# Kernel optimization log

Hardware: AMD Instinct MI355X
Metric: run time of the kernel (lower is better)

## Reference

```python
import jax, jax.numpy as jnp
import numpy as np

B, Hh, Ww, C = 2, 56, 56, 256
NH = 8
MH = MW = 7
NQ = 15


def setup_inputs() -> dict:
    key = jax.random.key(0)
    ks = jax.random.split(key, 8)
    x = jax.random.normal(ks[0], (B, Hh, Ww, C), jnp.float32)
    clstoken = jax.random.normal(ks[1], (B, NQ, C), jnp.float32)
    WN = MH * MW                      # 49 image windows
    WinPix = (Hh // MH) * (Ww // MW)  # 64 pixels per window
    clsWin = -(-NQ // WinPix)         # ceil -> 1 extra cls window
    M = WN + clsWin                   # 50
    # sparse top-k style routing mask; cls rows/cols all True (as in BiLayer)
    mask = jax.random.bernoulli(ks[2], 0.1, (B, M, M))
    mask = mask.at[:, WN:, :].set(True).at[:, :, WN:].set(True)
    mask = mask | jnp.eye(M, dtype=bool)[None]
    Wqkv = jax.random.normal(ks[3], (C, 3 * C), jnp.float32) * (C ** -0.5)
    bqkv = jnp.zeros((3 * C,), jnp.float32)
    lepe_w = jax.random.normal(ks[4], (3, 3, 1, C), jnp.float32) * 0.1  # depthwise HWIO
    lepe_b = jnp.zeros((C,), jnp.float32)
    Wo = jax.random.normal(ks[5], (C, C), jnp.float32) * (C ** -0.5)
    bo = jnp.zeros((C,), jnp.float32)
    return dict(x=x, clstoken=clstoken, mask=mask, Wqkv=Wqkv, bqkv=bqkv,
                lepe_w=lepe_w, lepe_b=lepe_b, Wo=Wo, bo=bo, mask_h=MH, mask_w=MW)


def reference(x, clstoken, mask, Wqkv, bqkv, lepe_w, lepe_b, Wo, bo, mask_h, mask_w):
    Bb, H, W, Cc = x.shape
    Nq = clstoken.shape[1]
    Nh = NH
    Hd = Cc // Nh
    Win_h, Win_w = H // mask_h, W // mask_w
    WinPix = Win_h * Win_w
    S_img = H * W
    S = S_img + Nq
    scale = Cc ** -0.5

    qkv = x @ Wqkv + bqkv
    q, k, v = jnp.split(qkv, 3, axis=-1)
    qkv_c = clstoken @ Wqkv + bqkv
    qc, kc, vc = jnp.split(qkv_c, 3, axis=-1)

    # depthwise lepe conv on v (NHWC)
    lepe = jax.lax.conv_general_dilated(
        v, lepe_w, (1, 1), 'SAME',
        dimension_numbers=('NHWC', 'HWIO', 'NHWC'),
        feature_group_count=Cc) + lepe_b

    def win(t):  # [B,H,W,C] -> [B,Nh,(j i h w),Hd] window-major token order
        t = t.reshape(Bb, mask_h, Win_h, mask_w, Win_w, Nh, Hd)
        return t.transpose(0, 5, 1, 3, 2, 4, 6).reshape(Bb, Nh, S_img, Hd)

    def heads_c(t):  # [B,Nq,C] -> [B,Nh,Nq,Hd]
        return t.reshape(Bb, Nq, Nh, Hd).transpose(0, 2, 1, 3)

    q = jnp.concatenate([win(q), heads_c(qc)], axis=2)
    k = jnp.concatenate([win(k), heads_c(kc)], axis=2)
    v = jnp.concatenate([win(v), heads_c(vc)], axis=2)

    # token-level mask from window-level routing mask: mask[b, q//WinPix, kv//WinPix]
    win_id = jnp.arange(S) // WinPix
    tokmask = mask[:, win_id[:, None], win_id[None, :]]  # [B,S,S]

    logits = jnp.einsum('bnqd,bnkd->bnqk', q, k) * scale
    logits = jnp.where(tokmask[:, None], logits, jnp.float32(-1e9))
    attn = jax.nn.softmax(logits, axis=-1)
    out = jnp.einsum('bnqk,bnkd->bnqd', attn, v)

    cls_out = out[:, :, S_img:, :].transpose(0, 2, 1, 3).reshape(Bb, Nq, Cc)
    ximg = out[:, :, :S_img, :].reshape(Bb, Nh, mask_h, mask_w, Win_h, Win_w, Hd)
    ximg = ximg.transpose(0, 2, 4, 3, 5, 1, 6).reshape(Bb, H, W, Cc)

    x_out = (ximg + lepe) @ Wo + bo
    cls_out = cls_out @ Wo + bo
    return (x_out, cls_out)
```

## Files before the change

kernel.cpp:

```cpp
#include <hip/hip_runtime.h>
#include <hip/hip_bf16.h>
#include <math.h>

#define Bsz 2
#define NHd 8
#define HD 32
#define CC 256
#define Himg 56
#define Wimg 56
#define SIMG 3136
#define NQtok 15
#define SS 3151
#define SP 3200
#define NWIN 50
#define WN 49
#define MM 50
#define MROWS (Bsz*SP)
#define NROWS (Bsz*SS)

#define QSZ (Bsz*NHd*SP*HD)
#define VSPSZ (Bsz*SIMG*CC)
#define ASZ (MROWS*CC)
#define WTSZ (768*CC)
#define WOTSZ (CC*CC)
#define USZ (MROWS*CC)

typedef __attribute__((ext_vector_type(8))) short bf16x8;
typedef __attribute__((ext_vector_type(4))) float f32x4;

__device__ __forceinline__ short f2bf(float f) {
    __hip_bfloat16 h = __float2bfloat16(f);
    return *reinterpret_cast<short*>(&h);
}
__device__ __forceinline__ float bf2f(short s) {
    unsigned int u = ((unsigned int)(unsigned short)s) << 16;
    return __uint_as_float(u);
}

__global__ __launch_bounds__(256) void prep_all(
        const float* __restrict__ x, const float* __restrict__ cls,
        const float* __restrict__ Wqkv, const float* __restrict__ Wo,
        const unsigned char* __restrict__ raw,
        short* __restrict__ Abf, short* __restrict__ Wt, short* __restrict__ Wot,
        unsigned char* __restrict__ mask8) {
    __shared__ __align__(16) float tile[64][65];
    int bid = blockIdx.x;
    int tid = threadIdx.x;
    if (bid < 800) {
        int idx = bid * 256 + tid;
        int row = idx >> 5;
        int c8 = (idx & 31) * 8;
        int b = row / SP, tok = row % SP;
        bf16x8 o = {0, 0, 0, 0, 0, 0, 0, 0};
        const float* p = nullptr;
        if (tok < SIMG)      p = x + (long)(b * SIMG + tok) * CC + c8;
        else if (tok < SS)   p = cls + (long)(b * NQtok + tok - SIMG) * CC + c8;
        if (p) {
            float4 a = *(const float4*)p, bb = *(const float4*)(p + 4);
            o[0] = f2bf(a.x); o[1] = f2bf(a.y); o[2] = f2bf(a.z); o[3] = f2bf(a.w);
            o[4] = f2bf(bb.x); o[5] = f2bf(bb.y); o[6] = f2bf(bb.z); o[7] = f2bf(bb.w);
        }
        *(bf16x8*)(Abf + (long)row * CC + c8) = o;
    } else if (bid < 864) {
        const float* src; short* dst; int srcld, k0, n0;
        if (bid < 848) {
            int b2 = bid - 800;
            k0 = (b2 & 3) * 64; n0 = (b2 >> 2) * 64;
            src = Wqkv; srcld = 768; dst = Wt;
        } else {
            int b2 = bid - 848;
            k0 = (b2 & 3) * 64; n0 = (b2 >> 2) * 64;
            src = Wo; srcld = 256; dst = Wot;
        }
        int c = tid & 63, r0 = tid >> 6;
        #pragma unroll
        for (int p = 0; p < 16; p++) {
            int kl = p * 4 + r0;
            tile[kl][c] = src[(long)(k0 + kl) * srcld + n0 + c];
        }
        __syncthreads();
        #pragma unroll
        for (int p = 0; p < 16; p++) {
            int nl = p * 4 + r0;
            dst[(long)(n0 + nl) * CC + k0 + c] = f2bf(tile[c][nl]);
        }
    } else {
        __shared__ int type_s;
        if (tid == 0) {
            int isbool = (raw[2453] | raw[2457] | raw[2461]) != 0;
            if (isbool) type_s = 0;
            else {
                unsigned int wd = *(const unsigned int*)(raw + 9800);
                type_s = (wd == 0x3F800000u) ? 2 : 1;
            }
        }
        __syncthreads();
        int t = type_s;
        for (int i = tid; i < Bsz * MM * MM; i += 256) {
            unsigned char v;
            if (t == 0) v = raw[i] ? 1 : 0;
            else v = (*(const unsigned int*)(raw + 4 * i)) ? 1 : 0;
            mask8[i] = v;
        }
    }
}

__global__ __launch_bounds__(256, 2) void qkv_gemm_mfma(
        const short* __restrict__ Abf, const short* __restrict__ Wt,
        const float* __restrict__ bqkv,
        short* __restrict__ Qbf, short* __restrict__ Kbf, short* __restrict__ Vtb,
        short* __restrict__ Vsp) {
    int tid = threadIdx.x;
    int w = tid >> 6, l = tid & 63, l15 = l & 15, hi = l >> 4;
    int row0 = blockIdx.x * 128 + w * 32;
    int n0 = blockIdx.y * 64;
    f32x4 acc[2][4];
    #pragma unroll
    for (int rs = 0; rs < 2; rs++)
        #pragma unroll
        for (int t = 0; t < 4; t++) acc[rs][t] = (f32x4){0.f, 0.f, 0.f, 0.f};
    const short* Ap0 = Abf + (long)(row0 + l15) * CC + hi * 8;
    const short* Ap1 = Ap0 + 16 * CC;
    const short* Bp = Wt + (long)(n0 + l15) * CC + hi * 8;
    #pragma unroll
    for (int k0 = 0; k0 < 256; k0 += 32) {
        bf16x8 a0 = *(const bf16x8*)(Ap0 + k0);
        bf16x8 a1 = *(const bf16x8*)(Ap1 + k0);
        #pragma unroll
        for (int t = 0; t < 4; t++) {
            bf16x8 bf = *(const bf16x8*)(Bp + t * 16 * CC + k0);
            acc[0][t] = __builtin_amdgcn_mfma_f32_16x16x32_bf16(a0, bf, acc[0][t], 0, 0, 0);
            acc[1][t] = __builtin_amdgcn_mfma_f32_16x16x32_bf16(a1, bf, acc[1][t], 0, 0, 0);
        }
    }
    float bias[4];
    #pragma unroll
    for (int t = 0; t < 4; t++) bias[t] = bqkv[n0 + t * 16 + l15];
    int which = n0 >> 8;
    #pragma unroll
    for (int rs = 0; rs < 2; rs++) {
        #pragma unroll
        for (int r = 0; r < 4; r++) {
            int row = row0 + rs * 16 + hi * 4 + r;
            int b = row / SP, tok = row % SP;
            int s;
            if (tok < SIMG) {
                int h = tok / Wimg, wq = tok % Wimg;
                s = (((h >> 3) * 7 + (wq >> 3)) << 6) | ((h & 7) << 3) | (wq & 7);
            } else s = tok;
            #pragma unroll
            for (int t = 0; t < 4; t++) {
                int n = n0 + t * 16 + l15;
                float v = acc[rs][t][r] + bias[t];
                int cch = n & 255;
                int head = cch >> 5, d = cch & 31;
                long off = (((long)(b * NHd + head)) * SP + s) * HD + d;
                if (which == 0)      Qbf[off] = f2bf(v * 0.0625f);
                else if (which == 1) Kbf[off] = f2bf(v);
                else {
                    short vb = f2bf(v);
                    Vtb[(((long)(b * NHd + head)) * NWIN + (s >> 6)) * 2048
                        + d * 64 + (s & 63)] = vb;
                    if (tok < SIMG) Vsp[(long)(b * SIMG + tok) * CC + cch] = vb;
                }
            }
        }
    }
}

__global__ __launch_bounds__(256, 2) void attn_mfma(
        const short* __restrict__ Qbf, const short* __restrict__ Kbf,
        const short* __restrict__ Vtb, const short* __restrict__ Vsp,
        const float* __restrict__ lepe_w, const float* __restrict__ lepe_b,
        const unsigned char* __restrict__ mask8,
        short* __restrict__ U) {
    __shared__ __align__(16) short Pl[4][16][72];
    __shared__ float Ms[4][16], Ls[4][16];
    __shared__ float MAcc[4][16][32];

    int qb = blockIdx.x % NWIN;
    int bh = blockIdx.x / NWIN;
    int b = bh >> 3, head = bh & 7;
    int tid = threadIdx.x;
    int w = tid >> 6;
    int l = tid & 63;
    int l15 = l & 15;
    int hi = l >> 4;
    bool is_cls = (qb == WN);
    int qrow0 = is_cls ? 0 : w * 16;

    bf16x8 qf = *(const bf16x8*)&Qbf[((long)bh * SP + qb * 64 + qrow0 + l15) * HD + hi * 8];

    f32x4 acc0 = {0.f, 0.f, 0.f, 0.f};
    f32x4 acc1 = {0.f, 0.f, 0.f, 0.f};
    float m_run[4], l_run[4];
    #pragma unroll
    for (int r = 0; r < 4; r++) { m_run[r] = -1e30f; l_run[r] = 0.f; }

    unsigned long long bits;
    if (!is_cls) {
        const unsigned char* mrow = mask8 + ((long)b * MM + qb) * MM;
        bits = __ballot(l < NWIN && mrow[l] != 0);
    } else {
        bits = (0x1111111111111ULL << w) & ((1ULL << 50) - 1);
    }

    int kb = __builtin_ctzll(bits);
    bits &= bits - 1;
    const short* Kp = Kbf + ((long)bh * SP + kb * 64) * HD + hi * 8;
    bf16x8 kc0 = *(const bf16x8*)(Kp + (0 * 16 + l15) * HD);
    bf16x8 kc1 = *(const bf16x8*)(Kp + (1 * 16 + l15) * HD);
    bf16x8 kc2 = *(const bf16x8*)(Kp + (2 * 16 + l15) * HD);
    bf16x8 kc3 = *(const bf16x8*)(Kp + (3 * 16 + l15) * HD);

    for (;;) {
        long kbase = ((long)bh * SP + kb * 64) * HD;
        const short* Vp = Vtb + kbase;
        bf16x8 va = *(const bf16x8*)&Vp[l15 * 64 + hi * 8];
        bf16x8 vb = *(const bf16x8*)&Vp[(16 + l15) * 64 + hi * 8];
        bf16x8 vc = *(const bf16x8*)&Vp[l15 * 64 + 32 + hi * 8];
        bf16x8 vd = *(const bf16x8*)&Vp[(16 + l15) * 64 + 32 + hi * 8];

        f32x4 s[4];
        {
            f32x4 z = {0.f, 0.f, 0.f, 0.f};
            s[0] = __builtin_amdgcn_mfma_f32_16x16x32_bf16(qf, kc0, z, 0, 0, 0);
            s[1] = __builtin_amdgcn_mfma_f32_16x16x32_bf16(qf, kc1, z, 0, 0, 0);
            s[2] = __builtin_amdgcn_mfma_f32_16x16x32_bf16(qf, kc2, z, 0, 0, 0);
            s[3] = __builtin_amdgcn_mfma_f32_16x16x32_bf16(qf, kc3, z, 0, 0, 0);
        }
        if (kb == WN) {
            #pragma unroll
            for (int t = 0; t < 4; t++)
                if (t * 16 + l15 >= NQtok) { s[t][0] = s[t][1] = s[t][2] = s[t][3] = -1e30f; }
        }

        int nkb = -1;
        bf16x8 kn0, kn1, kn2, kn3;
        if (bits) {
            nkb = __builtin_ctzll(bits);
            bits &= bits - 1;
            const short* Kn = Kbf + ((long)bh * SP + nkb * 64) * HD + hi * 8;
            kn0 = *(const bf16x8*)(Kn + (0 * 16 + l15) * HD);
            kn1 = *(const bf16x8*)(Kn + (1 * 16 + l15) * HD);
            kn2 = *(const bf16x8*)(Kn + (2 * 16 + l15) * HD);
            kn3 = *(const bf16x8*)(Kn + (3 * 16 + l15) * HD);
        }

        #pragma unroll
        for (int r = 0; r < 4; r++) {
            float pm = fmaxf(fmaxf(s[0][r], s[1][r]), fmaxf(s[2][r], s[3][r]));
            pm = fmaxf(pm, __shfl_xor(pm, 1));
            pm = fmaxf(pm, __shfl_xor(pm, 2));
            pm = fmaxf(pm, __shfl_xor(pm, 4));
            pm = fmaxf(pm, __shfl_xor(pm, 8));
            float mn = fmaxf(m_run[r], pm);
            float alpha = __expf(m_run[r] - mn);
            float ps = 0.f;
            #pragma unroll
            for (int t = 0; t < 4; t++) {
                float p = __expf(s[t][r] - mn);
                s[t][r] = p;
                ps += p;
            }
            ps += __shfl_xor(ps, 1);
            ps += __shfl_xor(ps, 2);
            ps += __shfl_xor(ps, 4);
            ps += __shfl_xor(ps, 8);
            l_run[r] = l_run[r] * alpha + ps;
            m_run[r] = mn;
            acc0[r] *= alpha;
            acc1[r] *= alpha;
            #pragma unroll
            for (int t = 0; t < 4; t++)
                Pl[w][hi * 4 + r][t * 16 + l15] = f2bf(s[t][r]);
        }
        bf16x8 pa0 = *(const bf16x8*)&Pl[w][l15][hi * 8];
        bf16x8 pa1 = *(const bf16x8*)&Pl[w][l15][32 + hi * 8];
        acc0 = __builtin_amdgcn_mfma_f32_16x16x32_bf16(pa0, va, acc0, 0, 0, 0);
        acc1 = __builtin_amdgcn_mfma_f32_16x16x32_bf16(pa0, vb, acc1, 0, 0, 0);
        acc0 = __builtin_amdgcn_mfma_f32_16x16x32_bf16(pa1, vc, acc0, 0, 0, 0);
        acc1 = __builtin_amdgcn_mfma_f32_16x16x32_bf16(pa1, vd, acc1, 0, 0, 0);

        if (nkb < 0) break;
        kb = nkb;
        kc0 = kn0; kc1 = kn1; kc2 = kn2; kc3 = kn3;
    }

    if (!is_cls) {
        float inv[4];
        #pragma unroll
        for (int r = 0; r < 4; r++) inv[r] = 1.f / l_run[r];
        int wh = (qb / 7) * 8, wwc = (qb % 7) * 8;
        #pragma unroll
        for (int half = 0; half < 2; half++) {
            int c = head * HD + half * 16 + l15;
            float lb = lepe_b[c];
            float lw[9];
            #pragma unroll
            for (int j = 0; j < 9; j++) lw[j] = lepe_w[j * CC + c];
            #pragma unroll
            for (int r = 0; r < 4; r++) {
                int inner = w * 16 + hi * 4 + r;
                int h0 = wh + (inner >> 3), w0 = wwc + (inner & 7);
                float u = (half ? acc1[r] : acc0[r]) * inv[r] + lb;
                #pragma unroll
                for (int dh = -1; dh <= 1; dh++) {
                    int h2 = h0 + dh;
                    if (h2 < 0 || h2 >= Himg) continue;
                    #pragma unroll
                    for (int dw = -1; dw <= 1; dw++) {
                        int w2 = w0 + dw;
                        if (w2 < 0 || w2 >= Wimg) continue;
                        u += bf2f(Vsp[((long)b * SIMG + h2 * Wimg + w2) * CC + c])
                           * lw[(dh + 1) * 3 + (dw + 1)];
                    }
                }
                U[((long)(b * SS + h0 * Wimg + w0)) * CC + c] = f2bf(u);
            }
        }
    } else {
        #pragma unroll
        for (int r = 0; r < 4; r++) {
            int row = hi * 4 + r;
            if (l15 == 0) { Ms[w][row] = m_run[r]; Ls[w][row] = l_run[r]; }
            MAcc[w][row][l15]      = acc0[r];
            MAcc[w][row][16 + l15] = acc1[r];
        }
        __syncthreads();
        if (w == 0) {
            #pragma unroll
            for (int r = 0; r < 4; r++) {
                int row = hi * 4 + r;
                if (row >= NQtok) continue;
                float M = fmaxf(fmaxf(Ms[0][row], Ms[1][row]),
                                fmaxf(Ms[2][row], Ms[3][row]));
                float L = 0.f, o0 = 0.f, o1 = 0.f;
                #pragma unroll
                for (int ww = 0; ww < 4; ww++) {
                    float sc = __expf(Ms[ww][row] - M);
                    L  += Ls[ww][row] * sc;
                    o0 += MAcc[ww][row][l15] * sc;
                    o1 += MAcc[ww][row][16 + l15] * sc;
                }
                float invL = 1.f / L;
                long urow = ((long)(b * SS + SIMG + row)) * CC + head * HD;
                U[urow + l15]      = f2bf(o0 * invL);
                U[urow + 16 + l15] = f2bf(o1 * invL);
            }
        }
    }
}

__global__ __launch_bounds__(256, 2) void out_gemm_mfma(
        const short* __restrict__ U, const short* __restrict__ Wot,
        const float* __restrict__ bo, float* __restrict__ out) {
    int tid = threadIdx.x;
    int w = tid >> 6, l = tid & 63, l15 = l & 15, hi = l >> 4;
    int row0 = blockIdx.x * 128 + w * 32;
    int n0 = blockIdx.y * 64;
    f32x4 acc[2][4];
    #pragma unroll
    for (int rs = 0; rs < 2; rs++)
        #pragma unroll
        for (int t = 0; t < 4; t++) acc[rs][t] = (f32x4){0.f, 0.f, 0.f, 0.f};
    const short* Ap0 = U + (long)(row0 + l15) * CC + hi * 8;
    const short* Ap1 = Ap0 + 16 * CC;
    const short* Bp = Wot + (long)(n0 + l15) * CC + hi * 8;
    #pragma unroll
    for (int k0 = 0; k0 < 256; k0 += 32) {
        bf16x8 a0 = *(const bf16x8*)(Ap0 + k0);
        bf16x8 a1 = *(const bf16x8*)(Ap1 + k0);
        #pragma unroll
        for (int t = 0; t < 4; t++) {
            bf16x8 bf = *(const bf16x8*)(Bp + t * 16 * CC + k0);
            acc[0][t] = __builtin_amdgcn_mfma_f32_16x16x32_bf16(a0, bf, acc[0][t], 0, 0, 0);
            acc[1][t] = __builtin_amdgcn_mfma_f32_16x16x32_bf16(a1, bf, acc[1][t], 0, 0, 0);
        }
    }
    float bias[4];
    #pragma unroll
    for (int t = 0; t < 4; t++) bias[t] = bo[n0 + t * 16 + l15];
    #pragma unroll
    for (int rs = 0; rs < 2; rs++) {
        #pragma unroll
        for (int r = 0; r < 4; r++) {
            int row = row0 + rs * 16 + hi * 4 + r;
            if (row >= NROWS) continue;
            int b = (row >= SS) ? 1 : 0;
            int tok = row - b * SS;
            long base;
            if (tok < SIMG) base = (long)(b * SIMG + tok) * CC;
            else base = (long)Bsz * SIMG * CC + (long)(b * NQtok + tok - SIMG) * CC;
            #pragma unroll
            for (int t = 0; t < 4; t++)
                out[base + n0 + t * 16 + l15] = acc[rs][t][r] + bias[t];
        }
    }
}

extern "C" void kernel_launch(void* const* d_in, const int* in_sizes, int n_in,
                              void* d_out, int out_size, void* d_ws, size_t ws_size,
                              hipStream_t stream) {
    const float* x      = (const float*)d_in[0];
    const float* cls    = (const float*)d_in[1];
    const unsigned char* mask_raw = (const unsigned char*)d_in[2];
    const float* Wqkv   = (const float*)d_in[3];
    const float* bqkv   = (const float*)d_in[4];
    const float* lepe_w = (const float*)d_in[5];
    const float* lepe_b = (const float*)d_in[6];
    const float* Wo     = (const float*)d_in[7];
    const float* bo     = (const float*)d_in[8];
    float* out = (float*)d_out;

    short* Qbf = (short*)d_ws;
    short* Kbf = Qbf + QSZ;
    short* Vtb = Kbf + QSZ;
    short* Abf = Vtb + QSZ;
    short* Wt  = Abf + ASZ;
    short* Wot = Wt + WTSZ;
    short* U   = Wot + WOTSZ;
    short* Vsp = U + USZ;
    unsigned char* mask8 = (unsigned char*)(Vsp + VSPSZ);

    prep_all<<<865, 256, 0, stream>>>(x, cls, Wqkv, Wo, mask_raw, Abf, Wt, Wot, mask8);
    qkv_gemm_mfma<<<dim3(MROWS / 128, 12), 256, 0, stream>>>(Abf, Wt, bqkv, Qbf, Kbf, Vtb, Vsp);
    attn_mfma<<<Bsz * NHd * NWIN, 256, 0, stream>>>(Qbf, Kbf, Vtb, Vsp, lepe_w, lepe_b, mask8, U);
    out_gemm_mfma<<<dim3(MROWS / 128, 4), 256, 0, stream>>>(U, Wot, bo, out);
}
```

Before: 82.87 us.

## Transpose attention MFMAs so each lane owns one query row

Swaps the MFMA operand order for QK^T and PV so the scores come out transposed. Each lane then holds one query row's values across its registers. The softmax row max and sum need only two cross-lane shuffles instead of four per row, with a single running max and sum per lane. P is written to LDS as packed bf16 pairs. The epilogue then loads LEPE weights and V neighbours as 4-wide vectors and stores U with ushort4. The cls-window merge path is rewritten to match the new lane mapping, which risks layout or indexing errors.

```diff
diff --git a/kernel.cpp b/kernel.cpp
--- a/kernel.cpp
+++ b/kernel.cpp
@@ -32,9 +32,13 @@
     __hip_bfloat16 h = __float2bfloat16(f);
     return *reinterpret_cast<short*>(&h);
 }
-__device__ __forceinline__ float bf2f(short s) {
-    unsigned int u = ((unsigned int)(unsigned short)s) << 16;
+__device__ __forceinline__ float bf2f(unsigned short s) {
+    unsigned int u = ((unsigned int)s) << 16;
     return __uint_as_float(u);
+}
+__device__ __forceinline__ unsigned int pk2(float lo, float hi) {
+    return ((unsigned int)(unsigned short)f2bf(hi) << 16)
+         | (unsigned int)(unsigned short)f2bf(lo);
 }
 
 __global__ __launch_bounds__(256) void prep_all(
@@ -174,7 +178,7 @@
         const float* __restrict__ lepe_w, const float* __restrict__ lepe_b,
         const unsigned char* __restrict__ mask8,
         short* __restrict__ U) {
-    __shared__ __align__(16) short Pl[4][16][72];
+    __shared__ __align__(16) unsigned int Pl[4][16][36];
     __shared__ float Ms[4][16], Ls[4][16];
     __shared__ float MAcc[4][16][32];
 
@@ -193,9 +197,7 @@
 
     f32x4 acc0 = {0.f, 0.f, 0.f, 0.f};
     f32x4 acc1 = {0.f, 0.f, 0.f, 0.f};
-    float m_run[4], l_run[4];
-    #pragma unroll
-    for (int r = 0; r < 4; r++) { m_run[r] = -1e30f; l_run[r] = 0.f; }
+    float m_run = -1e30f, l_run = 0.f;
 
     unsigned long long bits;
     if (!is_cls) {
@@ -224,15 +226,17 @@
         f32x4 s[4];
         {
             f32x4 z = {0.f, 0.f, 0.f, 0.f};
-            s[0] = __builtin_amdgcn_mfma_f32_16x16x32_bf16(qf, kc0, z, 0, 0, 0);
-            s[1] = __builtin_amdgcn_mfma_f32_16x16x32_bf16(qf, kc1, z, 0, 0, 0);
-            s[2] = __builtin_amdgcn_mfma_f32_16x16x32_bf16(qf, kc2, z, 0, 0, 0);
-            s[3] = __builtin_amdgcn_mfma_f32_16x16x32_bf16(qf, kc3, z, 0, 0, 0);
+            s[0] = __builtin_amdgcn_mfma_f32_16x16x32_bf16(kc0, qf, z, 0, 0, 0);
+            s[1] = __builtin_amdgcn_mfma_f32_16x16x32_bf16(kc1, qf, z, 0, 0, 0);
+            s[2] = __builtin_amdgcn_mfma_f32_16x16x32_bf16(kc2, qf, z, 0, 0, 0);
+            s[3] = __builtin_amdgcn_mfma_f32_16x16x32_bf16(kc3, qf, z, 0, 0, 0);
         }
         if (kb == WN) {
             #pragma unroll
             for (int t = 0; t < 4; t++)
-                if (t * 16 + l15 >= NQtok) { s[t][0] = s[t][1] = s[t][2] = s[t][3] = -1e30f; }
+                #pragma unroll
+                for (int r = 0; r < 4; r++)
+                    if (t * 16 + hi * 4 + r >= NQtok) s[t][r] = -1e30f;
         }
 
         int nkb = -1;
@@ -247,40 +251,46 @@
             kn3 = *(const bf16x8*)(Kn + (3 * 16 + l15) * HD);
         }
 
-        #pragma unroll
-        for (int r = 0; r < 4; r++) {
-            float pm = fmaxf(fmaxf(s[0][r], s[1][r]), fmaxf(s[2][r], s[3][r]));
-            pm = fmaxf(pm, __shfl_xor(pm, 1));
-            pm = fmaxf(pm, __shfl_xor(pm, 2));
-            pm = fmaxf(pm, __shfl_xor(pm, 4));
-            pm = fmaxf(pm, __shfl_xor(pm, 8));
-            float mn = fmaxf(m_run[r], pm);
-            float alpha = __expf(m_run[r] - mn);
-            float ps = 0.f;
-            #pragma unroll
-            for (int t = 0; t < 4; t++) {
+        float pm = fmaxf(fmaxf(s[0][0], s[0][1]), fmaxf(s[0][2], s[0][3]));
+        #pragma unroll
+        for (int t = 1; t < 4; t++) {
+            pm = fmaxf(pm, fmaxf(fmaxf(s[t][0], s[t][1]), fmaxf(s[t][2], s[t][3])));
+        }
+        pm = fmaxf(pm, __shfl_xor(pm, 16));
+        pm = fmaxf(pm, __shfl_xor(pm, 32));
+        float mn = fmaxf(m_run, pm);
+        float alpha = __expf(m_run - mn);
+        float ps = 0.f;
+        #pragma unroll
+        for (int t = 0; t < 4; t++) {
+            #pragma unroll
+            for (int r = 0; r < 4; r++) {
                 float p = __expf(s[t][r] - mn);
                 s[t][r] = p;
                 ps += p;
             }
-            ps += __shfl_xor(ps, 1);
-            ps += __shfl_xor(ps, 2);
-            ps += __shfl_xor(ps, 4);
-            ps += __shfl_xor(ps, 8);
-            l_run[r] = l_run[r] * alpha + ps;
-            m_run[r] = mn;
-            acc0[r] *= alpha;
-            acc1[r] *= alpha;
-            #pragma unroll
-            for (int t = 0; t < 4; t++)
-                Pl[w][hi * 4 + r][t * 16 + l15] = f2bf(s[t][r]);
-        }
-        bf16x8 pa0 = *(const bf16x8*)&Pl[w][l15][hi * 8];
-        bf16x8 pa1 = *(const bf16x8*)&Pl[w][l15][32 + hi * 8];
-        acc0 = __builtin_amdgcn_mfma_f32_16x16x32_bf16(pa0, va, acc0, 0, 0, 0);
-        acc1 = __builtin_amdgcn_mfma_f32_16x16x32_bf16(pa0, vb, acc1, 0, 0, 0);
-        acc0 = __builtin_amdgcn_mfma_f32_16x16x32_bf16(pa1, vc, acc0, 0, 0, 0);
-        acc1 = __builtin_amdgcn_mfma_f32_16x16x32_bf16(pa1, vd, acc1, 0, 0, 0);
+        }
+        ps += __shfl_xor(ps, 16);
+        ps += __shfl_xor(ps, 32);
+        l_run = l_run * alpha + ps;
+        m_run = mn;
+        #pragma unroll
+        for (int r = 0; r < 4; r++) { acc0[r] *= alpha; acc1[r] *= alpha; }
+
+        #pragma unroll
+        for (int t = 0; t < 4; t++) {
+            uint2 pw;
+            pw.x = pk2(s[t][0], s[t][1]);
+            pw.y = pk2(s[t][2], s[t][3]);
+            *(uint2*)&Pl[w][l15][t * 8 + hi * 2] = pw;
+        }
+        bf16x8 pb0 = *(const bf16x8*)&Pl[w][l15][hi * 4];
+        bf16x8 pb1 = *(const bf16x8*)&Pl[w][l15][16 + hi * 4];
+
+        acc0 = __builtin_amdgcn_mfma_f32_16x16x32_bf16(va, pb0, acc0, 0, 0, 0);
+        acc1 = __builtin_amdgcn_mfma_f32_16x16x32_bf16(vb, pb0, acc1, 0, 0, 0);
+        acc0 = __builtin_amdgcn_mfma_f32_16x16x32_bf16(vc, pb1, acc0, 0, 0, 0);
+        acc1 = __builtin_amdgcn_mfma_f32_16x16x32_bf16(vd, pb1, acc1, 0, 0, 0);
 
         if (nkb < 0) break;
         kb = nkb;
@@ -288,65 +298,82 @@
     }
 
     if (!is_cls) {
-        float inv[4];
-        #pragma unroll
-        for (int r = 0; r < 4; r++) inv[r] = 1.f / l_run[r];
+        float inv = 1.f / l_run;
         int wh = (qb / 7) * 8, wwc = (qb % 7) * 8;
-        #pragma unroll
-        for (int half = 0; half < 2; half++) {
-            int c = head * HD + half * 16 + l15;
-            float lb = lepe_b[c];
-            float lw[9];
-            #pragma unroll
-            for (int j = 0; j < 9; j++) lw[j] = lepe_w[j * CC + c];
-            #pragma unroll
-            for (int r = 0; r < 4; r++) {
-                int inner = w * 16 + hi * 4 + r;
-                int h0 = wh + (inner >> 3), w0 = wwc + (inner & 7);
-                float u = (half ? acc1[r] : acc0[r]) * inv[r] + lb;
-                #pragma unroll
-                for (int dh = -1; dh <= 1; dh++) {
-                    int h2 = h0 + dh;
-                    if (h2 < 0 || h2 >= Himg) continue;
-                    #pragma unroll
-                    for (int dw = -1; dw <= 1; dw++) {
-                        int w2 = w0 + dw;
-                        if (w2 < 0 || w2 >= Wimg) continue;
-                        u += bf2f(Vsp[((long)b * SIMG + h2 * Wimg + w2) * CC + c])
-                           * lw[(dh + 1) * 3 + (dw + 1)];
-                    }
-                }
-                U[((long)(b * SS + h0 * Wimg + w0)) * CC + c] = f2bf(u);
-            }
-        }
+        int inner = w * 16 + l15;
+        int h0 = wh + (inner >> 3), w0 = wwc + (inner & 7);
+        int c0 = head * HD + hi * 4;
+        float u0[4], u1[4];
+        #pragma unroll
+        for (int r = 0; r < 4; r++) {
+            u0[r] = acc0[r] * inv + lepe_b[c0 + r];
+            u1[r] = acc1[r] * inv + lepe_b[c0 + 16 + r];
+        }
+        #pragma unroll
+        for (int dh = -1; dh <= 1; dh++) {
+            int h2 = h0 + dh;
+            if (h2 < 0 || h2 >= Himg) continue;
+            #pragma unroll
+            for (int dw = -1; dw <= 1; dw++) {
+                int w2 = w0 + dw;
+                if (w2 < 0 || w2 >= Wimg) continue;
+                long vbase = ((long)b * SIMG + h2 * Wimg + w2) * CC;
+                int j = (dh + 1) * 3 + (dw + 1);
+                ushort4 v0 = *(const ushort4*)&Vsp[vbase + c0];
+                ushort4 v1 = *(const ushort4*)&Vsp[vbase + c0 + 16];
+                float4 g0 = *(const float4*)&lepe_w[j * CC + c0];
+                float4 g1 = *(const float4*)&lepe_w[j * CC + c0 + 16];
+                u0[0] += bf2f(v0.x) * g0.x; u0[1] += bf2f(v0.y) * g0.y;
+                u0[2] += bf2f(v0.z) * g0.z; u0[3] += bf2f(v0.w) * g0.w;
+                u1[0] += bf2f(v1.x) * g1.x; u1[1] += bf2f(v1.y) * g1.y;
+                u1[2] += bf2f(v1.z) * g1.z; u1[3] += bf2f(v1.w) * g1.w;
+            }
+        }
+        long ubase = ((long)(b * SS + h0 * Wimg + w0)) * CC + c0;
+        ushort4 o0, o1;
+        o0.x = (unsigned short)f2bf(u0[0]); o0.y = (unsigned short)f2bf(u0[1]);
+        o0.z = (unsigned short)f2bf(u0[2]); o0.w = (unsigned short)f2bf(u0[3]);
+        o1.x = (unsigned short)f2bf(u1[0]); o1.y = (unsigned short)f2bf(u1[1]);
+        o1.z = (unsigned short)f2bf(u1[2]); o1.w = (unsigned short)f2bf(u1[3]);
+        *(ushort4*)&U[ubase]      = o0;
+        *(ushort4*)&U[ubase + 16] = o1;
     } else {
+        if (hi == 0) { Ms[w][l15] = m_run; Ls[w][l15] = l_run; }
         #pragma unroll
         for (int r = 0; r < 4; r++) {
-            int row = hi * 4 + r;
-            if (l15 == 0) { Ms[w][row] = m_run[r]; Ls[w][row] = l_run[r]; }
-            MAcc[w][row][l15]      = acc0[r];
-            MAcc[w][row][16 + l15] = acc1[r];
+            MAcc[w][l15][hi * 4 + r]      = acc0[r];
+            MAcc[w][l15][16 + hi * 4 + r] = acc1[r];
         }
         __syncthreads();
         if (w == 0) {
-            #pragma unroll
-            for (int r = 0; r < 4; r++) {
-                int row = hi * 4 + r;
-                if (row >= NQtok) continue;
-                float M = fmaxf(fmaxf(Ms[0][row], Ms[1][row]),
-                                fmaxf(Ms[2][row], Ms[3][row]));
-                float L = 0.f, o0 = 0.f, o1 = 0.f;
+            float M = fmaxf(fmaxf(Ms[0][l15], Ms[1][l15]),
+                            fmaxf(Ms[2][l15], Ms[3][l15]));
+            float L = 0.f;
+            float o0[4] = {0.f, 0.f, 0.f, 0.f}, o1[4] = {0.f, 0.f, 0.f, 0.f};
+            #pragma unroll
+            for (int ww = 0; ww < 4; ww++) {
+                float sc = __expf(Ms[ww][l15] - M);
+                L += Ls[ww][l15] * sc;
                 #pragma unroll
-                for (int ww = 0; ww < 4; ww++) {
-                    float sc = __expf(Ms[ww][row] - M);
-                    L  += Ls[ww][row] * sc;
-                    o0 += MAcc[ww][row][l15] * sc;
-                    o1 += MAcc[ww][row][16 + l15] * sc;
+                for (int r = 0; r < 4; r++) {
+                    o0[r] += MAcc[ww][l15][hi * 4 + r] * sc;
+                    o1[r] += MAcc[ww][l15][16 + hi * 4 + r] * sc;
                 }
+            }
+            if (l15 < NQtok) {
                 float invL = 1.f / L;
-                long urow = ((long)(b * SS + SIMG + row)) * CC + head * HD;
-                U[urow + l15]      = f2bf(o0 * invL);
-                U[urow + 16 + l15] = f2bf(o1 * invL);
+                long ubase = ((long)(b * SS + SIMG + l15)) * CC + head * HD + hi * 4;
+                ushort4 q0, q1;
+                q0.x = (unsigned short)f2bf(o0[0] * invL);
+                q0.y = (unsigned short)f2bf(o0[1] * invL);
+                q0.z = (unsigned short)f2bf(o0[2] * invL);
+                q0.w = (unsigned short)f2bf(o0[3] * invL);
+                q1.x = (unsigned short)f2bf(o1[0] * invL);
+                q1.y = (unsigned short)f2bf(o1[1] * invL);
+                q1.z = (unsigned short)f2bf(o1[2] * invL);
+                q1.w = (unsigned short)f2bf(o1[3] * invL);
+                *(ushort4*)&U[ubase]      = q0;
+                *(ushort4*)&U[ubase + 16] = q1;
             }
         }
     }
```

Result: no change. 82.51 us (-0.4%).
